# Kernel tuning notes

Measured on AMD Instinct MI355X. Metric: run time of the kernel, lower is better.

Reference implementation:

```python
import jax, jax.numpy as jnp
import numpy as np

N, D, E, R, K = 8192, 1024, 8, 16, 2  # tokens, d_model, experts, lora rank, top_k


def setup_inputs() -> dict:
    key = jax.random.key(0)
    ks = jax.random.split(key, 6)
    s = 1.0 / np.sqrt(D)
    return {
        "x": jax.random.normal(ks[0], (N, D), jnp.float32),
        "W_gate": jax.random.normal(ks[1], (E, D), jnp.float32) * s,
        "A": jax.random.normal(ks[2], (E, D, R), jnp.float32) * s,
        "B": jax.random.normal(ks[3], (E, R, D), jnp.float32) * (1.0 / np.sqrt(R)),
        "W_base": jax.random.normal(ks[4], (D, D), jnp.float32) * s,
        "b_base": jax.random.normal(ks[5], (D,), jnp.float32) * 0.01,
    }


def reference(x, W_gate, A, B, W_base, b_base):
    # Gating: logits [N, E] -> top-k values/indices, softmax over the k slots
    logits = x @ W_gate.T
    topk_vals, topk_idx = jax.lax.top_k(logits, K)          # [N, K]
    w = jax.nn.softmax(topk_vals.astype(jnp.float32), axis=1).astype(x.dtype)
    # Dense combine weights [N, E]: weight for expert e if selected, else 0
    combine = jnp.sum(jax.nn.one_hot(topk_idx, E, dtype=x.dtype) * w[..., None], axis=1)
    # LoRA experts: expert_e(x) = x @ A_e @ B_e; weighted scatter-add fused via einsum
    h = jnp.einsum('nd,edr->enr', x, A)                     # [E, N, R]
    moe_out = jnp.einsum('enr,erd,ne->nd', h, B, combine)   # [N, D]
    # Base (shared) linear expert, always added when lora_experts=True
    base = x @ W_base.T + b_base
    return moe_out + base
```

## Files before the change

kernel.cpp:

```cpp
#include <hip/hip_runtime.h>
#include <stdint.h>

#define NTOK 8192
#define DM   1024
#define NE   8
#define NR   16
#define KX   1152

typedef short bf16x8 __attribute__((ext_vector_type(8)));
typedef float f32x4  __attribute__((ext_vector_type(4)));

__device__ __forceinline__ unsigned short f2bf(float f) {
    union { float f; unsigned u; } v; v.f = f;
    unsigned r = v.u + 0x7fffu + ((v.u >> 16) & 1u);
    return (unsigned short)(r >> 16);
}

__device__ __forceinline__ void gld16(const void* g, void* l) {
    __builtin_amdgcn_global_load_lds((__attribute__((address_space(1))) void*)g,
                                     (__attribute__((address_space(3))) void*)l,
                                     16, 0, 0);
}

__global__ __launch_bounds__(256) void prep(const float* __restrict__ x,
                                            const float* __restrict__ Wg,
                                            const float* __restrict__ Asrc,
                                            const float* __restrict__ Bsrc,
                                            const float* __restrict__ Wb,
                                            float* __restrict__ combine,
                                            unsigned short* __restrict__ Xext,
                                            unsigned short* __restrict__ WBext,
                                            unsigned short* __restrict__ At) {
    const int b = blockIdx.x;
    const int t = threadIdx.x;

    if (b < 2048) {
        const int lane = t & 63;
        const int w = t >> 6;
        const int n = b * 4 + w;

        const float4* x4 = (const float4*)(x + (size_t)n * DM);
        float4 xv[4];
        #pragma unroll
        for (int i = 0; i < 4; ++i) xv[i] = x4[i * 64 + lane];

        float acc[NE];
        #pragma unroll
        for (int e = 0; e < NE; ++e) {
            const float4* wg4 = (const float4*)(Wg + (size_t)e * DM);
            float s = 0.f;
            #pragma unroll
            for (int i = 0; i < 4; ++i) {
                float4 g = wg4[i * 64 + lane];
                s += xv[i].x * g.x + xv[i].y * g.y + xv[i].z * g.z + xv[i].w * g.w;
            }
            acc[e] = s;
        }
        #pragma unroll
        for (int off = 32; off >= 1; off >>= 1) {
            #pragma unroll
            for (int e = 0; e < NE; ++e) acc[e] += __shfl_xor(acc[e], off, 64);
        }
        float best = acc[0]; int bi = 0;
        #pragma unroll
        for (int e = 1; e < NE; ++e) if (acc[e] > best) { best = acc[e]; bi = e; }
        float sec = -1e30f; int si = 0;
        #pragma unroll
        for (int e = 0; e < NE; ++e) if (e != bi && acc[e] > sec) { sec = acc[e]; si = e; }
        const float ed = __expf(sec - best);
        const float w0 = 1.f / (1.f + ed);
        const float w1 = ed * w0;
        if (lane < NE)
            combine[n * NE + lane] = (lane == bi) ? w0 : ((lane == si) ? w1 : 0.f);

        unsigned short* xrow = Xext + (size_t)n * KX;
        #pragma unroll
        for (int i = 0; i < 4; ++i) {
            ushort4 o;
            o.x = f2bf(xv[i].x); o.y = f2bf(xv[i].y);
            o.z = f2bf(xv[i].z); o.w = f2bf(xv[i].w);
            *(ushort4*)(xrow + (i * 64 + lane) * 4) = o;
        }
    } else if (b < 3072) {
        const int j = b - 2048;
        unsigned short* row = WBext + (size_t)j * KX;
        float4 v = ((const float4*)(Wb + (size_t)j * DM))[t];
        ushort4 o;
        o.x = f2bf(v.x); o.y = f2bf(v.y); o.z = f2bf(v.z); o.w = f2bf(v.w);
        *(ushort4*)(row + t * 4) = o;
        if (t < 128) row[DM + t] = f2bf(Bsrc[(size_t)t * DM + j]);
    } else {
        const int p = b - 3072;
        const int e = p >> 4, r = p & 15;
        for (int d = t; d < DM; d += 256)
            At[(size_t)p * DM + d] = f2bf(Asrc[e * (DM * NR) + d * NR + r]);
    }
}

__global__ __launch_bounds__(256) void hall_kernel(unsigned short* Xext,
                                                   const unsigned short* __restrict__ At,
                                                   const float* __restrict__ combine) {
    __shared__ __align__(16) unsigned short lds[(32 + 128) * 64];
    const int t = threadIdx.x;
    const int lane = t & 63;
    const int w = t >> 6;
    const int quad = lane >> 4;
    const int l15 = lane & 15;
    const int bm = blockIdx.x;

    f32x4 acc[2][2] = {};
    const unsigned short* gA = Xext + (size_t)(bm * 32 + (t >> 3)) * KX + (t & 7) * 8;

    for (int k0 = 0; k0 < DM; k0 += 64) {
        __syncthreads();
        gld16(gA + k0, (char*)lds + w * 1024);
        #pragma unroll
        for (int r = 0; r < 4; ++r) {
            const unsigned short* g = At + (size_t)(r * 32 + (t >> 3)) * DM + k0 + (t & 7) * 8;
            gld16(g, (char*)lds + 4096 + r * 4096 + w * 1024);
        }
        __syncthreads();
        #pragma unroll
        for (int kk = 0; kk < 2; ++kk) {
            bf16x8 a[2], bb[2];
            #pragma unroll
            for (int i = 0; i < 2; ++i)
                a[i] = *(const bf16x8*)&lds[(i * 16 + l15) * 64 + kk * 32 + quad * 8];
            #pragma unroll
            for (int jf = 0; jf < 2; ++jf)
                bb[jf] = *(const bf16x8*)&lds[2048 + (w * 32 + jf * 16 + l15) * 64 + kk * 32 + quad * 8];
            #pragma unroll
            for (int i = 0; i < 2; ++i)
                #pragma unroll
                for (int jf = 0; jf < 2; ++jf)
                    acc[i][jf] = __builtin_amdgcn_mfma_f32_16x16x32_bf16(a[i], bb[jf], acc[i][jf], 0, 0, 0);
        }
    }
    #pragma unroll
    for (int i = 0; i < 2; ++i)
        #pragma unroll
        for (int jf = 0; jf < 2; ++jf) {
            const int p = w * 32 + jf * 16 + l15;
            const int e = p >> 4;
            #pragma unroll
            for (int v = 0; v < 4; ++v) {
                const int n = bm * 32 + i * 16 + quad * 4 + v;
                const float val = acc[i][jf][v] * combine[n * NE + e];
                Xext[(size_t)n * KX + DM + p] = f2bf(val);
            }
        }
}

__global__ __launch_bounds__(256) void mgemm(const unsigned short* __restrict__ Xext,
                                             const unsigned short* __restrict__ WBext,
                                             const float* __restrict__ bias,
                                             float* __restrict__ out) {
    __shared__ __align__(16) unsigned short lds[8192];
    const int t = threadIdx.x;
    const int lane = t & 63;
    const int w = t >> 6;
    const int quad = lane >> 4;
    const int l15 = lane & 15;

    const int bid = blockIdx.x;
    const int xcd = bid & 7;
    const int loc = bid >> 3;
    const int bm = xcd * 8 + (loc & 7);
    const int bn = loc >> 3;

    const int wm = (w & 1) * 64;
    const int wn = (w >> 1) * 64;

    f32x4 acc[4][4] = {};

    const unsigned short* gA0 = Xext  + (size_t)(bm * 128 +      (t >> 2)) * KX + (t & 3) * 8;
    const unsigned short* gA1 = Xext  + (size_t)(bm * 128 + 64 + (t >> 2)) * KX + (t & 3) * 8;
    const unsigned short* gB0 = WBext + (size_t)(bn * 128 +      (t >> 2)) * KX + (t & 3) * 8;
    const unsigned short* gB1 = WBext + (size_t)(bn * 128 + 64 + (t >> 2)) * KX + (t & 3) * 8;

    for (int k0 = 0; k0 < KX; k0 += 32) {
        __syncthreads();
        gld16(gA0 + k0, (char*)lds +           w * 1024);
        gld16(gA1 + k0, (char*)lds +  4096 +   w * 1024);
        gld16(gB0 + k0, (char*)lds +  8192 +   w * 1024);
        gld16(gB1 + k0, (char*)lds + 12288 +   w * 1024);
        __syncthreads();
        bf16x8 a[4], b[4];
        #pragma unroll
        for (int i = 0; i < 4; ++i)
            a[i] = *(const bf16x8*)&lds[(wm + i * 16 + l15) * 32 + quad * 8];
        #pragma unroll
        for (int j = 0; j < 4; ++j)
            b[j] = *(const bf16x8*)&lds[4096 + (wn + j * 16 + l15) * 32 + quad * 8];
        #pragma unroll
        for (int i = 0; i < 4; ++i)
            #pragma unroll
            for (int j = 0; j < 4; ++j)
                acc[i][j] = __builtin_amdgcn_mfma_f32_16x16x32_bf16(a[i], b[j], acc[i][j], 0, 0, 0);
    }

    #pragma unroll
    for (int j = 0; j < 4; ++j) {
        const int col = bn * 128 + wn + j * 16 + l15;
        const float bv = bias[col];
        #pragma unroll
        for (int i = 0; i < 4; ++i) {
            const int row = bm * 128 + wm + i * 16 + quad * 4;
            #pragma unroll
            for (int v = 0; v < 4; ++v)
                out[(size_t)(row + v) * DM + col] = acc[i][j][v] + bv;
        }
    }
}

extern "C" void kernel_launch(void* const* d_in, const int* in_sizes, int n_in,
                              void* d_out, int out_size, void* d_ws, size_t ws_size,
                              hipStream_t stream) {
    const float* x  = (const float*)d_in[0];
    const float* Wg = (const float*)d_in[1];
    const float* A  = (const float*)d_in[2];
    const float* B  = (const float*)d_in[3];
    const float* Wb = (const float*)d_in[4];
    const float* bb = (const float*)d_in[5];
    float* out = (float*)d_out;

    char* ws = (char*)d_ws;
    float*          combine = (float*)ws;
    unsigned short* Xext    = (unsigned short*)(ws + 262144);
    unsigned short* WBext   = (unsigned short*)(ws + 262144 + 18874368);
    unsigned short* At      = (unsigned short*)(ws + 262144 + 18874368 + 2359296);

    hipLaunchKernelGGL(prep,        dim3(3200), dim3(256), 0, stream,
                       x, Wg, A, B, Wb, combine, Xext, WBext, At);
    hipLaunchKernelGGL(hall_kernel, dim3(256),  dim3(256), 0, stream, Xext, At, combine);
    hipLaunchKernelGGL(mgemm,       dim3(512),  dim3(256), 0, stream, Xext, WBext, bb, out);
}
```

Baseline: 142.8 us.

## XOR-swizzle LDS tiles and double the K-step in mgemm

Applies an XOR swizzle to the 16-byte segments in global-to-LDS loads and in MFMA fragment reads, in both hall_kernel and mgemm, to cut LDS bank conflicts on the 64-element-wide rows. mgemm's K step goes from 32 to 64 and its LDS tile doubles, halving the number of barrier pairs per output tile. The larger LDS footprint may reduce occupancy, and there is still no double buffering.

```diff
diff --git a/kernel.cpp b/kernel.cpp
--- a/kernel.cpp
+++ b/kernel.cpp
@@ -108,27 +108,32 @@
     const int l15 = lane & 15;
     const int bm = blockIdx.x;
 
+    const int srow = t >> 3;
+    const int seg  = (t & 7) ^ (srow & 7);
+
     f32x4 acc[2][2] = {};
-    const unsigned short* gA = Xext + (size_t)(bm * 32 + (t >> 3)) * KX + (t & 7) * 8;
+    const unsigned short* gA = Xext + (size_t)(bm * 32 + srow) * KX + seg * 8;
 
     for (int k0 = 0; k0 < DM; k0 += 64) {
         __syncthreads();
         gld16(gA + k0, (char*)lds + w * 1024);
         #pragma unroll
         for (int r = 0; r < 4; ++r) {
-            const unsigned short* g = At + (size_t)(r * 32 + (t >> 3)) * DM + k0 + (t & 7) * 8;
+            const unsigned short* g = At + (size_t)(r * 32 + srow) * DM + k0 + seg * 8;
             gld16(g, (char*)lds + 4096 + r * 4096 + w * 1024);
         }
         __syncthreads();
         #pragma unroll
         for (int kk = 0; kk < 2; ++kk) {
+            const int gs = kk * 4 + quad;
+            const int sw = (gs ^ (l15 & 7)) * 8;
             bf16x8 a[2], bb[2];
             #pragma unroll
             for (int i = 0; i < 2; ++i)
-                a[i] = *(const bf16x8*)&lds[(i * 16 + l15) * 64 + kk * 32 + quad * 8];
+                a[i] = *(const bf16x8*)&lds[(i * 16 + l15) * 64 + sw];
             #pragma unroll
             for (int jf = 0; jf < 2; ++jf)
-                bb[jf] = *(const bf16x8*)&lds[2048 + (w * 32 + jf * 16 + l15) * 64 + kk * 32 + quad * 8];
+                bb[jf] = *(const bf16x8*)&lds[2048 + (w * 32 + jf * 16 + l15) * 64 + sw];
             #pragma unroll
             for (int i = 0; i < 2; ++i)
                 #pragma unroll
@@ -155,7 +160,7 @@
                                              const unsigned short* __restrict__ WBext,
                                              const float* __restrict__ bias,
                                              float* __restrict__ out) {
-    __shared__ __align__(16) unsigned short lds[8192];
+    __shared__ __align__(16) unsigned short lds[16384];
     const int t = threadIdx.x;
     const int lane = t & 63;
     const int w = t >> 6;
@@ -173,30 +178,38 @@
 
     f32x4 acc[4][4] = {};
 
-    const unsigned short* gA0 = Xext  + (size_t)(bm * 128 +      (t >> 2)) * KX + (t & 3) * 8;
-    const unsigned short* gA1 = Xext  + (size_t)(bm * 128 + 64 + (t >> 2)) * KX + (t & 3) * 8;
-    const unsigned short* gB0 = WBext + (size_t)(bn * 128 +      (t >> 2)) * KX + (t & 3) * 8;
-    const unsigned short* gB1 = WBext + (size_t)(bn * 128 + 64 + (t >> 2)) * KX + (t & 3) * 8;
-
-    for (int k0 = 0; k0 < KX; k0 += 32) {
-        __syncthreads();
-        gld16(gA0 + k0, (char*)lds +           w * 1024);
-        gld16(gA1 + k0, (char*)lds +  4096 +   w * 1024);
-        gld16(gB0 + k0, (char*)lds +  8192 +   w * 1024);
-        gld16(gB1 + k0, (char*)lds + 12288 +   w * 1024);
-        __syncthreads();
-        bf16x8 a[4], b[4];
-        #pragma unroll
-        for (int i = 0; i < 4; ++i)
-            a[i] = *(const bf16x8*)&lds[(wm + i * 16 + l15) * 32 + quad * 8];
-        #pragma unroll
-        for (int j = 0; j < 4; ++j)
-            b[j] = *(const bf16x8*)&lds[4096 + (wn + j * 16 + l15) * 32 + quad * 8];
-        #pragma unroll
-        for (int i = 0; i < 4; ++i)
+    const int srow = t >> 3;
+    const int seg  = (t & 7) ^ (srow & 7);
+    const unsigned short* gA = Xext  + (size_t)(bm * 128 + srow) * KX + seg * 8;
+    const unsigned short* gB = WBext + (size_t)(bn * 128 + srow) * KX + seg * 8;
+    char* ldsA = (char*)lds + w * 1024;
+    char* ldsB = (char*)lds + 16384 + w * 1024;
+
+    for (int k0 = 0; k0 < KX; k0 += 64) {
+        __syncthreads();
+        #pragma unroll
+        for (int c = 0; c < 4; ++c) {
+            gld16(gA + (size_t)c * 32 * KX + k0, ldsA + c * 4096);
+            gld16(gB + (size_t)c * 32 * KX + k0, ldsB + c * 4096);
+        }
+        __syncthreads();
+        #pragma unroll
+        for (int kk = 0; kk < 2; ++kk) {
+            const int gs = kk * 4 + quad;
+            const int sw = (gs ^ (l15 & 7)) * 8;
+            bf16x8 a[4], b[4];
+            #pragma unroll
+            for (int i = 0; i < 4; ++i)
+                a[i] = *(const bf16x8*)&lds[(wm + i * 16 + l15) * 64 + sw];
             #pragma unroll
             for (int j = 0; j < 4; ++j)
-                acc[i][j] = __builtin_amdgcn_mfma_f32_16x16x32_bf16(a[i], b[j], acc[i][j], 0, 0, 0);
+                b[j] = *(const bf16x8*)&lds[8192 + (wn + j * 16 + l15) * 64 + sw];
+            #pragma unroll
+            for (int i = 0; i < 4; ++i)
+                #pragma unroll
+                for (int j = 0; j < 4; ++j)
+                    acc[i][j] = __builtin_amdgcn_mfma_f32_16x16x32_bf16(a[i], b[j], acc[i][j], 0, 0, 0);
+        }
     }
 
     #pragma unroll
```

New measurement: 136.9 us. -4.1%, faster.
